# Optimization experiments

Measured on AMD Instinct MI355X. Metric: run time of the kernel, lower is better.

Reference implementation:

```python
import jax, jax.numpy as jnp
import numpy as np

B = 2          # batch of poses
H = 256        # detector height
W = 256        # detector width
NPTS = 128     # samples per ray (trilinear renderer)
DV = 256       # cubic CT volume side
SDD = 1020.0   # source-to-detector distance
DELX = 2.0     # detector pixel spacing (mm)


def setup_inputs() -> dict:
    key = jax.random.key(0)
    kd, kj = jax.random.split(key)
    density = jax.random.uniform(kd, (DV, DV, DV), dtype=jnp.float32)
    spacing = jnp.ones((3,), jnp.float32)
    origin = jnp.zeros((3,), jnp.float32)
    center = jnp.array([DV / 2.0, DV / 2.0, DV / 2.0], jnp.float32)
    # X-ray point source behind the volume, detector plane in front
    src = center + jnp.array([0.0, 0.0, -SDD / 2.0], jnp.float32)
    xs = (jnp.arange(W, dtype=jnp.float32) - W / 2.0 + 0.5) * DELX
    ys = (jnp.arange(H, dtype=jnp.float32) - H / 2.0 + 0.5) * DELX
    gy, gx = jnp.meshgrid(ys, xs, indexing='ij')
    tgt = jnp.stack([center[0] + gx, center[1] + gy,
                     jnp.full_like(gx, center[2] + SDD / 2.0)], axis=-1)
    target = jnp.broadcast_to(tgt.reshape(1, H * W, 3), (B, H * W, 3)) + jnp.zeros((B, 1, 3), jnp.float32)
    source = jnp.broadcast_to(src, (B, H * W, 3)) + 0.01 * jax.random.normal(kj, (B, 1, 3), jnp.float32)
    return {'source': source, 'target': target, 'density': density,
            'spacing': spacing, 'origin': origin, 'n_points': NPTS}


def _trilinear(vol, idx):
    """Trilinear interpolation of vol [D,H,W] at fractional voxel coords idx [...,3]; zero outside."""
    Dv, Hv, Wv = vol.shape
    f = jnp.floor(idx)
    w = idx - f                      # fractional part (differentiable wrt idx)
    fi = f.astype(jnp.int32)
    wx, wy, wz = w[..., 0], w[..., 1], w[..., 2]
    hi = jnp.array([Dv - 1, Hv - 1, Wv - 1], idx.dtype)
    inside = jnp.all((idx >= 0) & (idx <= hi), axis=-1)
    out = jnp.zeros(idx.shape[:-1], vol.dtype)
    for di in (0, 1):
        for dj in (0, 1):
            for dk in (0, 1):
                ci = jnp.clip(fi[..., 0] + di, 0, Dv - 1)
                cj = jnp.clip(fi[..., 1] + dj, 0, Hv - 1)
                ck = jnp.clip(fi[..., 2] + dk, 0, Wv - 1)
                wgt = (wx if di else 1.0 - wx) * (wy if dj else 1.0 - wy) * (wz if dk else 1.0 - wz)
                out = out + vol[ci, cj, ck] * wgt
    return out * inside.astype(vol.dtype)


def reference(source, target, density, spacing, origin, n_points):
    # Sample n_points equally spaced along each source->target ray
    t = jnp.linspace(0.0, 1.0, n_points, dtype=source.dtype)            # (S,)
    ray = target - source                                               # (B,N,3)
    pts = source[:, :, None, :] + t[None, None, :, None] * ray[:, :, None, :]  # (B,N,S,3)
    idx = (pts - origin) / spacing                                      # voxel coords
    vals = _trilinear(density, idx)                                     # (B,N,S)
    raylen = jnp.linalg.norm(ray, axis=-1)                              # (B,N)
    img = vals.sum(-1) * raylen / n_points                              # line integral
    Bsz = source.shape[0]
    return img.reshape(Bsz, 1, H, W)
```

## Files before the change

kernel.cpp:

```cpp
#include <hip/hip_runtime.h>

#define DVOX 256
#define HWSTRIDE (DVOX * DVOX)
#define IMG_W 256
#define IMG_H 256
#define TILE 16
#define NSPLIT 4

typedef float float2u __attribute__((ext_vector_type(2), aligned(4)));

__global__ __launch_bounds__(256) void drr_kernel(
    const float* __restrict__ source,
    const float* __restrict__ target,
    const float* __restrict__ density,
    const float* __restrict__ spacing,
    const float* __restrict__ origin,
    const int*   __restrict__ n_points,
    float* __restrict__ out)
{
    const int tx = threadIdx.x & (TILE - 1);
    const int ty = threadIdx.x / TILE;
    const int px = blockIdx.x * TILE + tx;
    const int py = blockIdx.y * TILE + ty;
    const int b     = blockIdx.z / NSPLIT;
    const int chunk = blockIdx.z % NSPLIT;
    const int gid = (b * IMG_H + py) * IMG_W + px;

    const int S = n_points[0];

    const float ox = origin[0], oy = origin[1], oz = origin[2];
    const float isx = 1.0f / spacing[0];
    const float isy = 1.0f / spacing[1];
    const float isz = 1.0f / spacing[2];

    const float sx = source[gid * 3 + 0];
    const float sy = source[gid * 3 + 1];
    const float sz = source[gid * 3 + 2];
    const float rx = target[gid * 3 + 0] - sx;
    const float ry = target[gid * 3 + 1] - sy;
    const float rz = target[gid * 3 + 2] - sz;

    const float px0 = (sx - ox) * isx;
    const float py0 = (sy - oy) * isy;
    const float pz0 = (sz - oz) * isz;
    const float dx = rx * isx;
    const float dy = ry * isy;
    const float dz = rz * isz;

    const float hi = (float)(DVOX - 1);

    float t_lo = 0.0f, t_hi = 1.0f;
    {
        if (fabsf(dx) < 1e-8f) {
            if (px0 < 0.0f || px0 > hi) { t_lo = 2.0f; t_hi = -2.0f; }
        } else {
            float inv = 1.0f / dx;
            float ta = (0.0f - px0) * inv, tb = (hi - px0) * inv;
            t_lo = fmaxf(t_lo, fminf(ta, tb));
            t_hi = fminf(t_hi, fmaxf(ta, tb));
        }
        if (fabsf(dy) < 1e-8f) {
            if (py0 < 0.0f || py0 > hi) { t_lo = 2.0f; t_hi = -2.0f; }
        } else {
            float inv = 1.0f / dy;
            float ta = (0.0f - py0) * inv, tb = (hi - py0) * inv;
            t_lo = fmaxf(t_lo, fminf(ta, tb));
            t_hi = fminf(t_hi, fmaxf(ta, tb));
        }
        if (fabsf(dz) < 1e-8f) {
            if (pz0 < 0.0f || pz0 > hi) { t_lo = 2.0f; t_hi = -2.0f; }
        } else {
            float inv = 1.0f / dz;
            float ta = (0.0f - pz0) * inv, tb = (hi - pz0) * inv;
            t_lo = fmaxf(t_lo, fminf(ta, tb));
            t_hi = fminf(t_hi, fmaxf(ta, tb));
        }
    }

    const float sm1 = (float)(S - 1);
    const float tstep = 1.0f / sm1;

    float acc = 0.0f;

    if (t_hi >= t_lo) {
        int s_lo = max(0, (int)floorf(t_lo * sm1) - 1);
        int s_hi = min(S - 1, (int)ceilf(t_hi * sm1) + 1);

        for (int s = s_lo + chunk; s <= s_hi; s += NSPLIT) {
            float t = (float)s * tstep;
            float x = fmaf(t, dx, px0);
            float y = fmaf(t, dy, py0);
            float z = fmaf(t, dz, pz0);

            if (x < 0.0f || x > hi || y < 0.0f || y > hi || z < 0.0f || z > hi)
                continue;

            int ix = min((int)x, DVOX - 2);
            int iy = min((int)y, DVOX - 2);
            int iz = min((int)z, DVOX - 2);
            float wx = x - (float)ix;
            float wy = y - (float)iy;
            float wz = z - (float)iz;

            const float* p00 = density + ((size_t)ix * HWSTRIDE + (size_t)iy * DVOX + iz);

            float2u v00 = *(const float2u*)(p00);
            float2u v01 = *(const float2u*)(p00 + DVOX);
            float2u v10 = *(const float2u*)(p00 + HWSTRIDE);
            float2u v11 = *(const float2u*)(p00 + HWSTRIDE + DVOX);

            float c00 = fmaf(wz, v00[1] - v00[0], v00[0]);
            float c01 = fmaf(wz, v01[1] - v01[0], v01[0]);
            float c10 = fmaf(wz, v10[1] - v10[0], v10[0]);
            float c11 = fmaf(wz, v11[1] - v11[0], v11[0]);
            float c0  = fmaf(wy, c01 - c00, c00);
            float c1  = fmaf(wy, c11 - c10, c10);
            acc += fmaf(wx, c1 - c0, c0);
        }
    }

    float raylen = sqrtf(rx * rx + ry * ry + rz * rz);
    atomicAdd(&out[gid], acc * raylen / (float)S);
}

extern "C" void kernel_launch(void* const* d_in, const int* in_sizes, int n_in,
                              void* d_out, int out_size, void* d_ws, size_t ws_size,
                              hipStream_t stream) {
    const float* source   = (const float*)d_in[0];
    const float* target   = (const float*)d_in[1];
    const float* density  = (const float*)d_in[2];
    const float* spacing  = (const float*)d_in[3];
    const float* origin   = (const float*)d_in[4];
    const int*   n_points = (const int*)d_in[5];
    float* out = (float*)d_out;

    int total = in_sizes[0] / 3;
    int B = total / (IMG_H * IMG_W);

    hipMemsetAsync(d_out, 0, (size_t)out_size * sizeof(float), stream);

    dim3 grid(IMG_W / TILE, IMG_H / TILE, B * NSPLIT);
    drr_kernel<<<grid, 256, 0, stream>>>(source, target, density, spacing,
                                         origin, n_points, out);
}
```

Measured before the change: 149.4 us.

## Repack density into z-major fp16 pair layout before ray marching

Adds a mask kernel that marks which z-slices any ray samples, and a repack kernel that rewrites those slices into a z-major layout. Each element stores the fp16 z-pairs for a voxel and its x-neighbour. A new ray-march kernel then reads two 8-byte words per sample instead of four strided float2 loads, so adjacent pixels touch adjacent memory. This removes the large-stride gathers of the original layout. In exchange, every call pays a full volume repack (read plus write of a larger buffer), and density loses precision by dropping to fp16.

```diff
diff --git a/kernel.cpp b/kernel.cpp
--- a/kernel.cpp
+++ b/kernel.cpp
@@ -1,4 +1,5 @@
 #include <hip/hip_runtime.h>
+#include <hip/hip_fp16.h>
 
 #define DVOX 256
 #define HWSTRIDE (DVOX * DVOX)
@@ -8,6 +9,206 @@
 #define NSPLIT 4
 
 typedef float float2u __attribute__((ext_vector_type(2), aligned(4)));
+
+#define MASK_OFF 0
+#define PK_OFF   4096
+#define PK_BYTES ((size_t)DVOX * DVOX * DVOX * 8)
+#define WS_NEED  (PK_OFF + PK_BYTES)
+
+__global__ __launch_bounds__(256) void mask_kernel(
+    const float* __restrict__ source,
+    const float* __restrict__ target,
+    const float* __restrict__ spacing,
+    const float* __restrict__ origin,
+    const int*   __restrict__ n_points,
+    unsigned int* __restrict__ gmask,
+    int total)
+{
+    __shared__ int lm[DVOX];
+    for (int i = threadIdx.x; i < DVOX; i += 256) lm[i] = 0;
+    __syncthreads();
+
+    const int S = n_points[0];
+    const float oz = origin[2];
+    const float isz = 1.0f / spacing[2];
+    const float tstep = 1.0f / (float)(S - 1);
+
+    int rays_per_block = (total + gridDim.x - 1) / gridDim.x;
+    int r0 = blockIdx.x * rays_per_block;
+    int r1 = min(r0 + rays_per_block, total);
+
+    for (int r = r0 + threadIdx.x; r < r1; r += 256) {
+        float sz = source[r * 3 + 2];
+        float tz = target[r * 3 + 2];
+        float pz0 = (sz - oz) * isz;
+        float dz  = (tz - sz) * isz;
+        for (int s = 0; s < S; ++s) {
+            float t = (float)s * tstep;
+            float z = fmaf(t, dz, pz0);
+            if (z >= 0.0f && z <= 255.0f) {
+                int iz = min((int)z, DVOX - 2);
+                lm[iz] = 1;
+            }
+        }
+    }
+    __syncthreads();
+    for (int i = threadIdx.x; i < DVOX; i += 256)
+        if (lm[i]) atomicOr(&gmask[i], 1u);
+}
+
+__global__ __launch_bounds__(256) void repack_kernel(
+    const float* __restrict__ density,
+    const unsigned int* __restrict__ gmask,
+    uint2* __restrict__ pk)
+{
+    const int p = blockIdx.z;
+    if (!gmask[p]) return;
+
+    const int x0 = blockIdx.x * TILE;
+    const int y0 = blockIdx.y * TILE;
+
+    __shared__ float2 sh[TILE * (TILE + 1)];
+
+    for (int l = threadIdx.x; l < (TILE + 1) * TILE; l += 256) {
+        int lx = l % (TILE + 1);
+        int ly = l / (TILE + 1);
+        int gx = min(x0 + lx, DVOX - 1);
+        int gy = y0 + ly;
+        const float* base = density + ((size_t)gx * HWSTRIDE + (size_t)gy * DVOX + p);
+        float2u v = *(const float2u*)base;
+        sh[ly * (TILE + 1) + lx] = make_float2(v[0], v[1]);
+    }
+    __syncthreads();
+
+    const int tx = threadIdx.x & (TILE - 1);
+    const int ty = threadIdx.x / TILE;
+    float2 s0 = sh[ty * (TILE + 1) + tx];
+    float2 s1 = sh[ty * (TILE + 1) + tx + 1];
+
+    __half2 lo = __floats2half2_rn(s0.x, s0.y);
+    __half2 hi = __floats2half2_rn(s1.x, s1.y);
+    uint2 w;
+    w.x = *(unsigned int*)&lo;
+    w.y = *(unsigned int*)&hi;
+
+    pk[((size_t)p * HWSTRIDE) + (size_t)(y0 + ty) * DVOX + (x0 + tx)] = w;
+}
+
+__global__ __launch_bounds__(256) void drr_fast_kernel(
+    const float* __restrict__ source,
+    const float* __restrict__ target,
+    const uint2* __restrict__ pk,
+    const float* __restrict__ spacing,
+    const float* __restrict__ origin,
+    const int*   __restrict__ n_points,
+    float* __restrict__ out)
+{
+    const int tx = threadIdx.x & (TILE - 1);
+    const int ty = threadIdx.x / TILE;
+    const int px = blockIdx.x * TILE + tx;
+    const int py = blockIdx.y * TILE + ty;
+    const int b     = blockIdx.z / NSPLIT;
+    const int chunk = blockIdx.z % NSPLIT;
+    const int gid = (b * IMG_H + py) * IMG_W + px;
+
+    const int S = n_points[0];
+
+    const float ox = origin[0], oy = origin[1], oz = origin[2];
+    const float isx = 1.0f / spacing[0];
+    const float isy = 1.0f / spacing[1];
+    const float isz = 1.0f / spacing[2];
+
+    const float sx = source[gid * 3 + 0];
+    const float sy = source[gid * 3 + 1];
+    const float sz = source[gid * 3 + 2];
+    const float rx = target[gid * 3 + 0] - sx;
+    const float ry = target[gid * 3 + 1] - sy;
+    const float rz = target[gid * 3 + 2] - sz;
+
+    const float px0 = (sx - ox) * isx;
+    const float py0 = (sy - oy) * isy;
+    const float pz0 = (sz - oz) * isz;
+    const float dx = rx * isx;
+    const float dy = ry * isy;
+    const float dz = rz * isz;
+
+    const float hi = (float)(DVOX - 1);
+
+    float t_lo = 0.0f, t_hi = 1.0f;
+    {
+        if (fabsf(dx) < 1e-8f) {
+            if (px0 < 0.0f || px0 > hi) { t_lo = 2.0f; t_hi = -2.0f; }
+        } else {
+            float inv = 1.0f / dx;
+            float ta = (0.0f - px0) * inv, tb = (hi - px0) * inv;
+            t_lo = fmaxf(t_lo, fminf(ta, tb));
+            t_hi = fminf(t_hi, fmaxf(ta, tb));
+        }
+        if (fabsf(dy) < 1e-8f) {
+            if (py0 < 0.0f || py0 > hi) { t_lo = 2.0f; t_hi = -2.0f; }
+        } else {
+            float inv = 1.0f / dy;
+            float ta = (0.0f - py0) * inv, tb = (hi - py0) * inv;
+            t_lo = fmaxf(t_lo, fminf(ta, tb));
+            t_hi = fminf(t_hi, fmaxf(ta, tb));
+        }
+        if (fabsf(dz) < 1e-8f) {
+            if (pz0 < 0.0f || pz0 > hi) { t_lo = 2.0f; t_hi = -2.0f; }
+        } else {
+            float inv = 1.0f / dz;
+            float ta = (0.0f - pz0) * inv, tb = (hi - pz0) * inv;
+            t_lo = fmaxf(t_lo, fminf(ta, tb));
+            t_hi = fminf(t_hi, fmaxf(ta, tb));
+        }
+    }
+
+    const float sm1 = (float)(S - 1);
+    const float tstep = 1.0f / sm1;
+
+    float acc = 0.0f;
+
+    if (t_hi >= t_lo) {
+        int s_lo = max(0, (int)floorf(t_lo * sm1) - 1);
+        int s_hi = min(S - 1, (int)ceilf(t_hi * sm1) + 1);
+
+        for (int s = s_lo + chunk; s <= s_hi; s += NSPLIT) {
+            float t = (float)s * tstep;
+            float x = fmaf(t, dx, px0);
+            float y = fmaf(t, dy, py0);
+            float z = fmaf(t, dz, pz0);
+
+            if (x < 0.0f || x > hi || y < 0.0f || y > hi || z < 0.0f || z > hi)
+                continue;
+
+            int ix = min((int)x, DVOX - 2);
+            int iy = min((int)y, DVOX - 2);
+            int iz = min((int)z, DVOX - 2);
+            float wx = x - (float)ix;
+            float wy = y - (float)iy;
+            float wz = z - (float)iz;
+
+            size_t eidx = (size_t)iz * HWSTRIDE + (size_t)iy * DVOX + ix;
+            uint2 e0 = pk[eidx];
+            uint2 e1 = pk[eidx + DVOX];
+
+            float2 f00 = __half22float2(*(__half2*)&e0.x);
+            float2 f10 = __half22float2(*(__half2*)&e0.y);
+            float2 f01 = __half22float2(*(__half2*)&e1.x);
+            float2 f11 = __half22float2(*(__half2*)&e1.y);
+
+            float c00 = fmaf(wz, f00.y - f00.x, f00.x);
+            float c10 = fmaf(wz, f10.y - f10.x, f10.x);
+            float c01 = fmaf(wz, f01.y - f01.x, f01.x);
+            float c11 = fmaf(wz, f11.y - f11.x, f11.x);
+            float c0  = fmaf(wy, c01 - c00, c00);
+            float c1  = fmaf(wy, c11 - c10, c10);
+            acc += fmaf(wx, c1 - c0, c0);
+        }
+    }
+
+    float raylen = sqrtf(rx * rx + ry * ry + rz * rz);
+    atomicAdd(&out[gid], acc * raylen / (float)S);
+}
 
 __global__ __launch_bounds__(256) void drr_kernel(
     const float* __restrict__ source,
@@ -27,7 +228,6 @@
     const int gid = (b * IMG_H + py) * IMG_W + px;
 
     const int S = n_points[0];
-
     const float ox = origin[0], oy = origin[1], oz = origin[2];
     const float isx = 1.0f / spacing[0];
     const float isy = 1.0f / spacing[1];
@@ -43,72 +243,42 @@
     const float px0 = (sx - ox) * isx;
     const float py0 = (sy - oy) * isy;
     const float pz0 = (sz - oz) * isz;
-    const float dx = rx * isx;
-    const float dy = ry * isy;
-    const float dz = rz * isz;
-
+    const float dx = rx * isx, dy = ry * isy, dz = rz * isz;
     const float hi = (float)(DVOX - 1);
 
     float t_lo = 0.0f, t_hi = 1.0f;
-    {
-        if (fabsf(dx) < 1e-8f) {
-            if (px0 < 0.0f || px0 > hi) { t_lo = 2.0f; t_hi = -2.0f; }
-        } else {
-            float inv = 1.0f / dx;
-            float ta = (0.0f - px0) * inv, tb = (hi - px0) * inv;
-            t_lo = fmaxf(t_lo, fminf(ta, tb));
-            t_hi = fminf(t_hi, fmaxf(ta, tb));
-        }
-        if (fabsf(dy) < 1e-8f) {
-            if (py0 < 0.0f || py0 > hi) { t_lo = 2.0f; t_hi = -2.0f; }
-        } else {
-            float inv = 1.0f / dy;
-            float ta = (0.0f - py0) * inv, tb = (hi - py0) * inv;
-            t_lo = fmaxf(t_lo, fminf(ta, tb));
-            t_hi = fminf(t_hi, fmaxf(ta, tb));
-        }
-        if (fabsf(dz) < 1e-8f) {
-            if (pz0 < 0.0f || pz0 > hi) { t_lo = 2.0f; t_hi = -2.0f; }
-        } else {
-            float inv = 1.0f / dz;
-            float ta = (0.0f - pz0) * inv, tb = (hi - pz0) * inv;
-            t_lo = fmaxf(t_lo, fminf(ta, tb));
-            t_hi = fminf(t_hi, fmaxf(ta, tb));
-        }
-    }
+    if (fabsf(dx) < 1e-8f) { if (px0 < 0.0f || px0 > hi) { t_lo = 2.0f; t_hi = -2.0f; } }
+    else { float inv = 1.0f / dx; float ta = -px0 * inv, tb = (hi - px0) * inv;
+           t_lo = fmaxf(t_lo, fminf(ta, tb)); t_hi = fminf(t_hi, fmaxf(ta, tb)); }
+    if (fabsf(dy) < 1e-8f) { if (py0 < 0.0f || py0 > hi) { t_lo = 2.0f; t_hi = -2.0f; } }
+    else { float inv = 1.0f / dy; float ta = -py0 * inv, tb = (hi - py0) * inv;
+           t_lo = fmaxf(t_lo, fminf(ta, tb)); t_hi = fminf(t_hi, fmaxf(ta, tb)); }
+    if (fabsf(dz) < 1e-8f) { if (pz0 < 0.0f || pz0 > hi) { t_lo = 2.0f; t_hi = -2.0f; } }
+    else { float inv = 1.0f / dz; float ta = -pz0 * inv, tb = (hi - pz0) * inv;
+           t_lo = fmaxf(t_lo, fminf(ta, tb)); t_hi = fminf(t_hi, fmaxf(ta, tb)); }
 
     const float sm1 = (float)(S - 1);
     const float tstep = 1.0f / sm1;
-
     float acc = 0.0f;
 
     if (t_hi >= t_lo) {
         int s_lo = max(0, (int)floorf(t_lo * sm1) - 1);
         int s_hi = min(S - 1, (int)ceilf(t_hi * sm1) + 1);
-
         for (int s = s_lo + chunk; s <= s_hi; s += NSPLIT) {
             float t = (float)s * tstep;
             float x = fmaf(t, dx, px0);
             float y = fmaf(t, dy, py0);
             float z = fmaf(t, dz, pz0);
-
-            if (x < 0.0f || x > hi || y < 0.0f || y > hi || z < 0.0f || z > hi)
-                continue;
-
+            if (x < 0.0f || x > hi || y < 0.0f || y > hi || z < 0.0f || z > hi) continue;
             int ix = min((int)x, DVOX - 2);
             int iy = min((int)y, DVOX - 2);
             int iz = min((int)z, DVOX - 2);
-            float wx = x - (float)ix;
-            float wy = y - (float)iy;
-            float wz = z - (float)iz;
-
+            float wx = x - (float)ix, wy = y - (float)iy, wz = z - (float)iz;
             const float* p00 = density + ((size_t)ix * HWSTRIDE + (size_t)iy * DVOX + iz);
-
             float2u v00 = *(const float2u*)(p00);
             float2u v01 = *(const float2u*)(p00 + DVOX);
             float2u v10 = *(const float2u*)(p00 + HWSTRIDE);
             float2u v11 = *(const float2u*)(p00 + HWSTRIDE + DVOX);
-
             float c00 = fmaf(wz, v00[1] - v00[0], v00[0]);
             float c01 = fmaf(wz, v01[1] - v01[0], v01[0]);
             float c10 = fmaf(wz, v10[1] - v10[0], v10[0]);
@@ -118,7 +288,6 @@
             acc += fmaf(wx, c1 - c0, c0);
         }
     }
-
     float raylen = sqrtf(rx * rx + ry * ry + rz * rz);
     atomicAdd(&out[gid], acc * raylen / (float)S);
 }
@@ -139,7 +308,24 @@
 
     hipMemsetAsync(d_out, 0, (size_t)out_size * sizeof(float), stream);
 
-    dim3 grid(IMG_W / TILE, IMG_H / TILE, B * NSPLIT);
-    drr_kernel<<<grid, 256, 0, stream>>>(source, target, density, spacing,
-                                         origin, n_points, out);
-}
+    if (ws_size >= WS_NEED) {
+        unsigned int* gmask = (unsigned int*)((char*)d_ws + MASK_OFF);
+        uint2* pk = (uint2*)((char*)d_ws + PK_OFF);
+
+        hipMemsetAsync(gmask, 0, DVOX * sizeof(unsigned int), stream);
+
+        mask_kernel<<<256, 256, 0, stream>>>(source, target, spacing, origin,
+                                             n_points, gmask, total);
+
+        dim3 rgrid(DVOX / TILE, DVOX / TILE, DVOX - 1);
+        repack_kernel<<<rgrid, 256, 0, stream>>>(density, gmask, pk);
+
+        dim3 grid(IMG_W / TILE, IMG_H / TILE, B * NSPLIT);
+        drr_fast_kernel<<<grid, 256, 0, stream>>>(source, target, pk, spacing,
+                                                  origin, n_points, out);
+    } else {
+        dim3 grid(IMG_W / TILE, IMG_H / TILE, B * NSPLIT);
+        drr_kernel<<<grid, 256, 0, stream>>>(source, target, density, spacing,
+                                             origin, n_points, out);
+    }
+}
```

Measured after the change: 147.3 us. No clear change (-1.4%).
